# Kernel optimization log

Measured on AMD Instinct MI355X. Metric: run time of the kernel, lower is better.

Reference implementation:

```python
import jax, jax.numpy as jnp
import numpy as np

N, E, H, C = 100000, 800000, 128, 26


def setup_inputs() -> dict:
    key = jax.random.key(0)
    ks = jax.random.split(key, 12)
    s = 0.05
    return {
        "node_feat": jax.random.normal(ks[0], (N, H), jnp.float32),
        "descriptor": jax.random.normal(ks[1], (N, H), jnp.float32),
        "sub_idx": jax.random.randint(ks[2], (E,), 0, N, jnp.int32),
        "obj_idx": jax.random.randint(ks[3], (E,), 0, N, jnp.int32),
        "We": jax.random.normal(ks[4], (2 * H, H), jnp.float32) * s,
        "be": jnp.zeros((H,), jnp.float32),
        "Wq": jax.random.normal(ks[5], (2 * H, H), jnp.float32) * s,
        "bq": jnp.zeros((H,), jnp.float32),
        "Wk": jax.random.normal(ks[6], (2 * H, H), jnp.float32) * s,
        "bk": jnp.zeros((H,), jnp.float32),
        "Wv": jax.random.normal(ks[7], (2 * H, H), jnp.float32) * s,
        "bv": jnp.zeros((H,), jnp.float32),
        "Wc1": jax.random.normal(ks[8], (H, H // 2), jnp.float32) * s,
        "bc1": jnp.zeros((H // 2,), jnp.float32),
        "Wc2": jax.random.normal(ks[9], (H // 2, H // 4), jnp.float32) * s,
        "bc2": jnp.zeros((H // 4,), jnp.float32),
        "Wc3": jax.random.normal(ks[10], (H // 4, C), jnp.float32) * s,
        "bc3": jnp.zeros((C,), jnp.float32),
    }


def reference(node_feat, descriptor, sub_idx, obj_idx,
              We, be, Wq, bq, Wk, bk, Wv, bv,
              Wc1, bc1, Wc2, bc2, Wc3, bc3):
    # Gather edge endpoint features (irregular access), concat -> [E, 2H]
    geo = jnp.concatenate([node_feat[sub_idx], node_feat[obj_idx]], axis=1)
    non_geo = jnp.concatenate([descriptor[sub_idx], descriptor[obj_idx]], axis=1)

    origin = geo @ We + be          # edge_lin
    query = geo @ Wq + bq
    key = non_geo @ Wk + bk
    value = non_geo @ Wv + bv

    # elementwise q*k then softmax over feature dim (dim=1 in torch)
    alpha = jax.nn.softmax(query * key, axis=1)
    fused = value * alpha + origin  # [E, H]

    # classifier: Linear+ReLU, Linear (no ReLU), Linear(->classes)
    h = jax.nn.relu(fused @ Wc1 + bc1)
    h = h @ Wc2 + bc2
    out = h @ Wc3 + bc3             # [E, C]
    return out
```

## Files before the change

### kernel.cpp

```cpp
#include <hip/hip_runtime.h>
#include <hip/hip_bf16.h>

typedef short short8 __attribute__((ext_vector_type(8)));
typedef float f32x4 __attribute__((ext_vector_type(4)));
typedef unsigned int uint4v __attribute__((ext_vector_type(4)));

#define NEDGE 800000
#define NNODE 100000
#define HD    128
#define TM    64
#define LDA   264
#define LDF   136
#define LDH1  72
#define LDH2  40

#define WOFF_NFB   142336
#define WOFF_DESCB (142336 + 12800000)
#define WS_NEED    ((size_t)(142336 + 2 * 12800000) * 2)

__device__ __forceinline__ unsigned short f2bf(float f) {
    unsigned int u = __float_as_uint(f);
    unsigned int r = u + 0x7fffu + ((u >> 16) & 1u);
    return (unsigned short)(r >> 16);
}
__device__ __forceinline__ float bf2f(unsigned short u) {
    union { unsigned int i; float f; } v; v.i = ((unsigned int)u) << 16; return v.f;
}
__device__ __forceinline__ unsigned int pk_bf16(float a, float b) {
    __hip_bfloat162 h = __float22bfloat162_rn(make_float2(a, b));
    union { __hip_bfloat162 h2; unsigned int u; } c; c.h2 = h; return c.u;
}

__global__ void pack_convert(const float* __restrict__ We, const float* __restrict__ Wq,
                             const float* __restrict__ Wk, const float* __restrict__ Wv,
                             const float* __restrict__ Wc1, const float* __restrict__ Wc2,
                             const float* __restrict__ Wc3,
                             const float* __restrict__ nf, const float* __restrict__ desc,
                             unsigned short* __restrict__ ws) {
    int b = blockIdx.x;
    if (b >= 556) {
        int cb = b - 556;
        const float* src; unsigned short* dst;
        if (cb < 6250) { src = nf;   dst = ws + WOFF_NFB; }
        else           { src = desc; dst = ws + WOFF_DESCB; cb -= 6250; }
        long i = ((long)cb * 256 + threadIdx.x) * 8;
        f32x4 v0 = *(const f32x4*)(src + i);
        f32x4 v1 = *(const f32x4*)(src + i + 4);
        uint4v o;
        o.x = pk_bf16(v0[0], v0[1]);
        o.y = pk_bf16(v0[2], v0[3]);
        o.z = pk_bf16(v1[0], v1[1]);
        o.w = pk_bf16(v1[2], v1[3]);
        *(uint4v*)(dst + i) = o;
        return;
    }
    const float* src; unsigned short* dst; int KT, NT, ncols;
    if (b < 512) {
        int sel = b >> 7;
        src = sel == 0 ? We : sel == 1 ? Wq : sel == 2 ? Wk : Wv;
        dst = ws + sel * 32768;
        KT = 8; NT = 8; ncols = 128; b &= 127;
    } else if (b < 544) { src = Wc1; dst = ws + 131072; KT = 4; NT = 4; ncols = 64; b -= 512; }
    else if (b < 552)   { src = Wc2; dst = ws + 139264; KT = 2; NT = 2; ncols = 32; b -= 544; }
    else                { src = Wc3; dst = ws + 141312; KT = 1; NT = 2; ncols = 26; b -= 552; }
    int idx = b * 256 + threadIdx.x;
    int total = NT * KT * 64 * 8;
    if (idx >= total) return;
    int j = idx & 7;
    int l = (idx >> 3) & 63;
    int rem = idx >> 9;
    int s = rem % KT;
    int t = rem / KT;
    int k = s * 32 + ((l >> 4) << 3) + j;
    int n = t * 16 + (l & 15);
    dst[idx] = (n < ncols) ? f2bf(src[k * ncols + n]) : (unsigned short)0;
}

template<bool TAB>
__global__ __launch_bounds__(256, 4)
void fused_relcls(const float* __restrict__ nf,
                  const float* __restrict__ desc,
                  const int* __restrict__ sub, const int* __restrict__ obj,
                  const unsigned short* __restrict__ nfb, const unsigned short* __restrict__ descb,
                  const unsigned short* __restrict__ wef, const unsigned short* __restrict__ wqf,
                  const unsigned short* __restrict__ wkf, const unsigned short* __restrict__ wvf,
                  const unsigned short* __restrict__ wc1f, const unsigned short* __restrict__ wc2f,
                  const unsigned short* __restrict__ wc3f,
                  const float* __restrict__ be, const float* __restrict__ bq,
                  const float* __restrict__ bk, const float* __restrict__ bv,
                  const float* __restrict__ bc1, const float* __restrict__ bc2,
                  const float* __restrict__ bc3,
                  float* __restrict__ out)
{
    __shared__ __align__(16) unsigned short Abuf[TM * LDA];
    __shared__ float ssm[TM * 4];
    unsigned short* h1Buf = Abuf + 8704;
    unsigned short* h2Buf = Abuf + 13312;

    const int t  = threadIdx.x;
    const int w  = t >> 6;
    const int l  = t & 63;
    const int cl = l & 15;
    const int cq = l >> 4;
    const long e0 = (long)blockIdx.x * TM;
    const int wu = __builtin_amdgcn_readfirstlane(w);
    const int half = l >> 5;
    const int ci   = l & 31;

    if constexpr (TAB) {
        #pragma unroll
        for (int i = 0; i < 16; ++i) {
            int e = wu + 4 * i;
            int idx = half ? obj[e0 + e] : sub[e0 + e];
            uint2 g = *(const uint2*)(nfb + (long)idx * HD + ci * 4);
            *(uint2*)&Abuf[e * LDA + half * HD + ci * 4] = g;
        }
    } else {
        #pragma unroll
        for (int i = 0; i < 16; ++i) {
            int e = wu + 4 * i;
            int si = sub[e0 + e];
            int oi = obj[e0 + e];
            int idx = half ? oi : si;
            f32x4 v = *(const f32x4*)(nf + (long)idx * HD + ci * 4);
            uint2 o;
            o.x = pk_bf16(v[0], v[1]);
            o.y = pk_bf16(v[2], v[3]);
            *(uint2*)&Abuf[e * LDA + half * HD + ci * 4] = o;
        }
    }
    __syncthreads();

    f32x4 acc0[4][2], acc1[4][2];
    unsigned int opk[16];

    {
        float b0 = be[w * 32 + cl], b1 = be[w * 32 + 16 + cl];
        #pragma unroll
        for (int m = 0; m < 4; ++m) {
            acc0[m][0] = (f32x4){b0, b0, b0, b0};
            acc0[m][1] = (f32x4){b1, b1, b1, b1};
        }
        #pragma unroll
        for (int ks = 0; ks < 8; ++ks) {
            short8 a[4];
            #pragma unroll
            for (int m = 0; m < 4; ++m)
                a[m] = *(const short8*)&Abuf[(m * 16 + cl) * LDA + ks * 32 + cq * 8];
            short8 bw[2];
            #pragma unroll
            for (int tt = 0; tt < 2; ++tt)
                bw[tt] = *(const short8*)&wef[(((w * 2 + tt) * 8 + ks) * 64 + l) * 8];
            #pragma unroll
            for (int m = 0; m < 4; ++m)
                #pragma unroll
                for (int tt = 0; tt < 2; ++tt)
                    acc0[m][tt] = __builtin_amdgcn_mfma_f32_16x16x32_bf16(a[m], bw[tt], acc0[m][tt], 0, 0, 0);
        }
        #pragma unroll
        for (int m = 0; m < 4; ++m)
            #pragma unroll
            for (int tt = 0; tt < 2; ++tt) {
                opk[m * 4 + tt * 2 + 0] = pk_bf16(acc0[m][tt][0], acc0[m][tt][1]);
                opk[m * 4 + tt * 2 + 1] = pk_bf16(acc0[m][tt][2], acc0[m][tt][3]);
            }
    }

    {
        float b0 = bq[w * 32 + cl], b1 = bq[w * 32 + 16 + cl];
        #pragma unroll
        for (int m = 0; m < 4; ++m) {
            acc0[m][0] = (f32x4){b0, b0, b0, b0};
            acc0[m][1] = (f32x4){b1, b1, b1, b1};
        }
        #pragma unroll
        for (int ks = 0; ks < 8; ++ks) {
            short8 a[4];
            #pragma unroll
            for (int m = 0; m < 4; ++m)
                a[m] = *(const short8*)&Abuf[(m * 16 + cl) * LDA + ks * 32 + cq * 8];
            short8 bw[2];
            #pragma unroll
            for (int tt = 0; tt < 2; ++tt)
                bw[tt] = *(const short8*)&wqf[(((w * 2 + tt) * 8 + ks) * 64 + l) * 8];
            #pragma unroll
            for (int m = 0; m < 4; ++m)
                #pragma unroll
                for (int tt = 0; tt < 2; ++tt)
                    acc0[m][tt] = __builtin_amdgcn_mfma_f32_16x16x32_bf16(a[m], bw[tt], acc0[m][tt], 0, 0, 0);
        }
    }
    __syncthreads();

    if constexpr (TAB) {
        #pragma unroll
        for (int i = 0; i < 16; ++i) {
            int e = wu + 4 * i;
            int idx = half ? obj[e0 + e] : sub[e0 + e];
            uint2 g = *(const uint2*)(descb + (long)idx * HD + ci * 4);
            *(uint2*)&Abuf[e * LDA + half * HD + ci * 4] = g;
        }
    } else {
        #pragma unroll
        for (int i = 0; i < 16; ++i) {
            int e = wu + 4 * i;
            int si = sub[e0 + e];
            int oi = obj[e0 + e];
            int idx = half ? oi : si;
            f32x4 v = *(const f32x4*)(desc + (long)idx * HD + ci * 4);
            uint2 o;
            o.x = pk_bf16(v[0], v[1]);
            o.y = pk_bf16(v[2], v[3]);
            *(uint2*)&Abuf[e * LDA + half * HD + ci * 4] = o;
        }
    }
    __syncthreads();

    {
        float b0 = bk[w * 32 + cl], b1 = bk[w * 32 + 16 + cl];
        #pragma unroll
        for (int m = 0; m < 4; ++m) {
            acc1[m][0] = (f32x4){b0, b0, b0, b0};
            acc1[m][1] = (f32x4){b1, b1, b1, b1};
        }
        #pragma unroll
        for (int ks = 0; ks < 8; ++ks) {
            short8 a[4];
            #pragma unroll
            for (int m = 0; m < 4; ++m)
                a[m] = *(const short8*)&Abuf[(m * 16 + cl) * LDA + ks * 32 + cq * 8];
            short8 bw[2];
            #pragma unroll
            for (int tt = 0; tt < 2; ++tt)
                bw[tt] = *(const short8*)&wkf[(((w * 2 + tt) * 8 + ks) * 64 + l) * 8];
            #pragma unroll
            for (int m = 0; m < 4; ++m)
                #pragma unroll
                for (int tt = 0; tt < 2; ++tt)
                    acc1[m][tt] = __builtin_amdgcn_mfma_f32_16x16x32_bf16(a[m], bw[tt], acc1[m][tt], 0, 0, 0);
        }
        #pragma unroll
        for (int m = 0; m < 4; ++m)
            #pragma unroll
            for (int tt = 0; tt < 2; ++tt)
                acc0[m][tt] *= acc1[m][tt];
    }

    {
        #pragma unroll
        for (int m = 0; m < 4; ++m) {
            float es[4];
            #pragma unroll
            for (int r = 0; r < 4; ++r) {
                float ea = __expf(acc0[m][0][r]);
                float eb = __expf(acc0[m][1][r]);
                acc0[m][0][r] = ea;
                acc0[m][1][r] = eb;
                float s = ea + eb;
                s += __shfl_xor(s, 1);
                s += __shfl_xor(s, 2);
                s += __shfl_xor(s, 4);
                s += __shfl_xor(s, 8);
                es[r] = s;
            }
            if (cl == 0) {
                #pragma unroll
                for (int r = 0; r < 4; ++r)
                    ssm[(m * 16 + cq * 4 + r) * 4 + w] = es[r];
            }
        }
    }

    {
        float b0 = bv[w * 32 + cl], b1 = bv[w * 32 + 16 + cl];
        #pragma unroll
        for (int m = 0; m < 4; ++m) {
            acc1[m][0] = (f32x4){b0, b0, b0, b0};
            acc1[m][1] = (f32x4){b1, b1, b1, b1};
        }
        #pragma unroll
        for (int ks = 0; ks < 8; ++ks) {
            short8 a[4];
            #pragma unroll
            for (int m = 0; m < 4; ++m)
                a[m] = *(const short8*)&Abuf[(m * 16 + cl) * LDA + ks * 32 + cq * 8];
            short8 bw[2];
            #pragma unroll
            for (int tt = 0; tt < 2; ++tt)
                bw[tt] = *(const short8*)&wvf[(((w * 2 + tt) * 8 + ks) * 64 + l) * 8];
            #pragma unroll
            for (int m = 0; m < 4; ++m)
                #pragma unroll
                for (int tt = 0; tt < 2; ++tt)
                    acc1[m][tt] = __builtin_amdgcn_mfma_f32_16x16x32_bf16(a[m], bw[tt], acc1[m][tt], 0, 0, 0);
        }
    }
    __syncthreads();

    {
        unsigned short* fusedBuf = Abuf;
        #pragma unroll
        for (int m = 0; m < 4; ++m)
            #pragma unroll
            for (int r = 0; r < 4; ++r) {
                int row = m * 16 + cq * 4 + r;
                f32x4 b = *(const f32x4*)&ssm[row * 4];
                float inv = 1.0f / (b[0] + b[1] + b[2] + b[3]);
                #pragma unroll
                for (int tt = 0; tt < 2; ++tt) {
                    unsigned int word = opk[m * 4 + tt * 2 + (r >> 1)];
                    unsigned short us = (r & 1) ? (unsigned short)(word >> 16) : (unsigned short)(word & 0xffffu);
                    float Oval = bf2f(us);
                    float alpha = acc0[m][tt][r] * inv;
                    float f = acc1[m][tt][r] * alpha + Oval;
                    fusedBuf[row * LDF + w * 32 + tt * 16 + cl] = f2bf(f);
                }
            }
    }
    __syncthreads();

    {
        const unsigned short* fusedBuf = Abuf;
        float b1 = bc1[w * 16 + cl];
        f32x4 acc[4];
        #pragma unroll
        for (int m = 0; m < 4; ++m) acc[m] = (f32x4){b1, b1, b1, b1};
        #pragma unroll
        for (int ks = 0; ks < 4; ++ks) {
            short8 a[4];
            #pragma unroll
            for (int m = 0; m < 4; ++m)
                a[m] = *(const short8*)&fusedBuf[(m * 16 + cl) * LDF + ks * 32 + cq * 8];
            short8 bw = *(const short8*)&wc1f[((w * 4 + ks) * 64 + l) * 8];
            #pragma unroll
            for (int m = 0; m < 4; ++m)
                acc[m] = __builtin_amdgcn_mfma_f32_16x16x32_bf16(a[m], bw, acc[m], 0, 0, 0);
        }
        #pragma unroll
        for (int m = 0; m < 4; ++m)
            #pragma unroll
            for (int r = 0; r < 4; ++r)
                h1Buf[(m * 16 + cq * 4 + r) * LDH1 + w * 16 + cl] = f2bf(fmaxf(acc[m][r], 0.f));
    }
    __syncthreads();

    {
        int tn = w & 1, mh = w >> 1;
        float b2 = bc2[tn * 16 + cl];
        f32x4 acc[2];
        acc[0] = (f32x4){b2, b2, b2, b2};
        acc[1] = (f32x4){b2, b2, b2, b2};
        #pragma unroll
        for (int ks = 0; ks < 2; ++ks) {
            short8 a[2];
            #pragma unroll
            for (int mm = 0; mm < 2; ++mm)
                a[mm] = *(const short8*)&h1Buf[((mh * 2 + mm) * 16 + cl) * LDH1 + ks * 32 + cq * 8];
            short8 bw = *(const short8*)&wc2f[((tn * 2 + ks) * 64 + l) * 8];
            #pragma unroll
            for (int mm = 0; mm < 2; ++mm)
                acc[mm] = __builtin_amdgcn_mfma_f32_16x16x32_bf16(a[mm], bw, acc[mm], 0, 0, 0);
        }
        #pragma unroll
        for (int mm = 0; mm < 2; ++mm)
            #pragma unroll
            for (int r = 0; r < 4; ++r)
                h2Buf[((mh * 2 + mm) * 16 + cq * 4 + r) * LDH2 + tn * 16 + cl] = f2bf(acc[mm][r]);
    }
    __syncthreads();

    {
        f32x4 acc[2];
        #pragma unroll
        for (int tt = 0; tt < 2; ++tt) {
            int col = tt * 16 + cl;
            float b3 = (col < 26) ? bc3[col] : 0.f;
            acc[tt] = (f32x4){b3, b3, b3, b3};
        }
        short8 a = *(const short8*)&h2Buf[(w * 16 + cl) * LDH2 + cq * 8];
        #pragma unroll
        for (int tt = 0; tt < 2; ++tt)
            acc[tt] = __builtin_amdgcn_mfma_f32_16x16x32_bf16(a, *(const short8*)&wc3f[(tt * 64 + l) * 8], acc[tt], 0, 0, 0);
        float* ostg = (float*)Abuf;
        #pragma unroll
        for (int tt = 0; tt < 2; ++tt) {
            int col = tt * 16 + cl;
            if (col < 26) {
                #pragma unroll
                for (int r = 0; r < 4; ++r)
                    ostg[(w * 16 + cq * 4 + r) * 26 + col] = acc[tt][r];
            }
        }
    }
    __syncthreads();

    {
        const uint4v* src = (const uint4v*)Abuf;
        uint4v* dst = (uint4v*)(out + e0 * 26);
        #pragma unroll
        for (int k2 = 0; k2 < 2; ++k2) {
            int idx = t + k2 * 256;
            if (idx < 416)
                dst[idx] = src[idx];
        }
    }
}

extern "C" void kernel_launch(void* const* d_in, const int* in_sizes, int n_in,
                              void* d_out, int out_size, void* d_ws, size_t ws_size,
                              hipStream_t stream) {
    const float* nf   = (const float*)d_in[0];
    const float* desc = (const float*)d_in[1];
    const int* sub = (const int*)d_in[2];
    const int* obj = (const int*)d_in[3];
    const float* We  = (const float*)d_in[4];
    const float* be  = (const float*)d_in[5];
    const float* Wq  = (const float*)d_in[6];
    const float* bq  = (const float*)d_in[7];
    const float* Wk  = (const float*)d_in[8];
    const float* bk  = (const float*)d_in[9];
    const float* Wv  = (const float*)d_in[10];
    const float* bv  = (const float*)d_in[11];
    const float* Wc1 = (const float*)d_in[12];
    const float* bc1 = (const float*)d_in[13];
    const float* Wc2 = (const float*)d_in[14];
    const float* bc2 = (const float*)d_in[15];
    const float* Wc3 = (const float*)d_in[16];
    const float* bc3 = (const float*)d_in[17];

    unsigned short* ws = (unsigned short*)d_ws;
    unsigned short* wef  = ws;
    unsigned short* wqf  = ws + 32768;
    unsigned short* wkf  = ws + 65536;
    unsigned short* wvf  = ws + 98304;
    unsigned short* wc1f = ws + 131072;
    unsigned short* wc2f = ws + 139264;
    unsigned short* wc3f = ws + 141312;
    unsigned short* nfb   = ws + WOFF_NFB;
    unsigned short* descb = ws + WOFF_DESCB;

    const bool tab = (ws_size >= WS_NEED);
    const int prep_grid = tab ? 13056 : 556;

    pack_convert<<<prep_grid, 256, 0, stream>>>(We, Wq, Wk, Wv, Wc1, Wc2, Wc3, nf, desc, ws);

    if (tab) {
        fused_relcls<true><<<NEDGE / TM, 256, 0, stream>>>(
            nf, desc, sub, obj, nfb, descb,
            wef, wqf, wkf, wvf, wc1f, wc2f, wc3f,
            be, bq, bk, bv, bc1, bc2, bc3,
            (float*)d_out);
    } else {
        fused_relcls<false><<<NEDGE / TM, 256, 0, stream>>>(
            nf, desc, sub, obj, nfb, descb,
            wef, wqf, wkf, wvf, wc1f, wc2f, wc3f,
            be, bq, bk, bv, bc1, bc2, bc3,
            (float*)d_out);
    }
}
```

Before: 513.1 us.

## Persistent grid with register prefetch of next tile's gathers and paired MFMA passes

Turns the fused edge kernel into a persistent kernel with a fixed grid that loops over tiles. The next tile's bf16 node_feat and descriptor rows are prefetched into registers while the current tile computes, so gather latency overlaps with MFMA work. Both feature sets are staged in one wider LDS buffer, and the E/Q and K/V projections are computed in paired passes, which removes the mid-kernel reload and barriers. The cost is more registers (occupancy hint lowered from 4 to 2 blocks), more LDS, and a pack kernel that launches twice as many blocks with half the work each.

```diff
diff --git a/kernel.cpp b/kernel.cpp
--- a/kernel.cpp
+++ b/kernel.cpp
@@ -9,10 +9,9 @@
 #define NNODE 100000
 #define HD    128
 #define TM    64
-#define LDA   264
-#define LDF   136
-#define LDH1  72
-#define LDH2  40
+#define NTILES (NEDGE / TM)
+#define GRID_P 1024
+#define LDA2  528
 
 #define WOFF_NFB   142336
 #define WOFF_DESCB (142336 + 12800000)
@@ -41,17 +40,14 @@
     if (b >= 556) {
         int cb = b - 556;
         const float* src; unsigned short* dst;
-        if (cb < 6250) { src = nf;   dst = ws + WOFF_NFB; }
-        else           { src = desc; dst = ws + WOFF_DESCB; cb -= 6250; }
-        long i = ((long)cb * 256 + threadIdx.x) * 8;
-        f32x4 v0 = *(const f32x4*)(src + i);
-        f32x4 v1 = *(const f32x4*)(src + i + 4);
-        uint4v o;
-        o.x = pk_bf16(v0[0], v0[1]);
-        o.y = pk_bf16(v0[2], v0[3]);
-        o.z = pk_bf16(v1[0], v1[1]);
-        o.w = pk_bf16(v1[2], v1[3]);
-        *(uint4v*)(dst + i) = o;
+        if (cb < 12500) { src = nf;   dst = ws + WOFF_NFB; }
+        else            { src = desc; dst = ws + WOFF_DESCB; cb -= 12500; }
+        long i = ((long)cb * 256 + threadIdx.x) * 4;
+        f32x4 v = *(const f32x4*)(src + i);
+        uint2 o;
+        o.x = pk_bf16(v[0], v[1]);
+        o.y = pk_bf16(v[2], v[3]);
+        *(uint2*)(dst + i) = o;
         return;
     }
     const float* src; unsigned short* dst; int KT, NT, ncols;
@@ -77,7 +73,7 @@
 }
 
 template<bool TAB>
-__global__ __launch_bounds__(256, 4)
+__global__ __launch_bounds__(256, 2)
 void fused_relcls(const float* __restrict__ nf,
                   const float* __restrict__ desc,
                   const int* __restrict__ sub, const int* __restrict__ obj,
@@ -92,317 +88,279 @@
                   const float* __restrict__ bc3,
                   float* __restrict__ out)
 {
-    __shared__ __align__(16) unsigned short Abuf[TM * LDA];
+    __shared__ __align__(16) unsigned short Abuf[TM * LDA2];
+    __shared__ __align__(16) unsigned short h2s[TM * 40];
+    __shared__ __align__(16) float ostg[TM * 26];
     __shared__ float ssm[TM * 4];
-    unsigned short* h1Buf = Abuf + 8704;
-    unsigned short* h2Buf = Abuf + 13312;
 
     const int t  = threadIdx.x;
     const int w  = t >> 6;
     const int l  = t & 63;
     const int cl = l & 15;
     const int cq = l >> 4;
-    const long e0 = (long)blockIdx.x * TM;
     const int wu = __builtin_amdgcn_readfirstlane(w);
     const int half = l >> 5;
     const int ci   = l & 31;
 
+    const float bO0 = be[w * 32 + cl], bO1 = be[w * 32 + 16 + cl];
+    const float bQ0 = bq[w * 32 + cl], bQ1 = bq[w * 32 + 16 + cl];
+    const float bK0 = bk[w * 32 + cl], bK1 = bk[w * 32 + 16 + cl];
+    const float bV0 = bv[w * 32 + cl], bV1 = bv[w * 32 + 16 + cl];
+    const float bC1 = bc1[w * 16 + cl];
+    const int   tn = w & 1, mh = w >> 1;
+    const float bC2 = bc2[tn * 16 + cl];
+    const int   col0 = cl, col1 = 16 + cl;
+    const float bC3a = bc3[col0];
+    const float bC3b = (col1 < 26) ? bc3[col1] : 0.f;
+
+    uint2 pre[32];
+
     if constexpr (TAB) {
+        long pe0 = (long)blockIdx.x * TM;
         #pragma unroll
         for (int i = 0; i < 16; ++i) {
             int e = wu + 4 * i;
-            int idx = half ? obj[e0 + e] : sub[e0 + e];
-            uint2 g = *(const uint2*)(nfb + (long)idx * HD + ci * 4);
-            *(uint2*)&Abuf[e * LDA + half * HD + ci * 4] = g;
-        }
-    } else {
-        #pragma unroll
-        for (int i = 0; i < 16; ++i) {
-            int e = wu + 4 * i;
-            int si = sub[e0 + e];
-            int oi = obj[e0 + e];
-            int idx = half ? oi : si;
-            f32x4 v = *(const f32x4*)(nf + (long)idx * HD + ci * 4);
-            uint2 o;
-            o.x = pk_bf16(v[0], v[1]);
-            o.y = pk_bf16(v[2], v[3]);
-            *(uint2*)&Abuf[e * LDA + half * HD + ci * 4] = o;
+            int idx = half ? obj[pe0 + e] : sub[pe0 + e];
+            pre[i]      = *(const uint2*)(nfb   + (long)idx * HD + ci * 4);
+            pre[16 + i] = *(const uint2*)(descb + (long)idx * HD + ci * 4);
         }
     }
-    __syncthreads();
-
-    f32x4 acc0[4][2], acc1[4][2];
-    unsigned int opk[16];
-
-    {
-        float b0 = be[w * 32 + cl], b1 = be[w * 32 + 16 + cl];
-        #pragma unroll
-        for (int m = 0; m < 4; ++m) {
-            acc0[m][0] = (f32x4){b0, b0, b0, b0};
-            acc0[m][1] = (f32x4){b1, b1, b1, b1};
-        }
-        #pragma unroll
-        for (int ks = 0; ks < 8; ++ks) {
-            short8 a[4];
+
+    for (int tile = blockIdx.x; tile < NTILES; tile += GRID_P) {
+        const long e0 = (long)tile * TM;
+
+        if constexpr (TAB) {
+            #pragma unroll
+            for (int i = 0; i < 16; ++i) {
+                int e = wu + 4 * i;
+                *(uint2*)&Abuf[e * LDA2 + half * HD + ci * 4]       = pre[i];
+                *(uint2*)&Abuf[e * LDA2 + 256 + half * HD + ci * 4] = pre[16 + i];
+            }
+        } else {
+            #pragma unroll
+            for (int i = 0; i < 16; ++i) {
+                int e = wu + 4 * i;
+                int idx = half ? obj[e0 + e] : sub[e0 + e];
+                f32x4 v = *(const f32x4*)(nf + (long)idx * HD + ci * 4);
+                uint2 o; o.x = pk_bf16(v[0], v[1]); o.y = pk_bf16(v[2], v[3]);
+                *(uint2*)&Abuf[e * LDA2 + half * HD + ci * 4] = o;
+                f32x4 v2 = *(const f32x4*)(desc + (long)idx * HD + ci * 4);
+                uint2 o2; o2.x = pk_bf16(v2[0], v2[1]); o2.y = pk_bf16(v2[2], v2[3]);
+                *(uint2*)&Abuf[e * LDA2 + 256 + half * HD + ci * 4] = o2;
+            }
+        }
+        __syncthreads();
+
+        if constexpr (TAB) {
+            int ptile = (tile + GRID_P < NTILES) ? (tile + GRID_P) : tile;
+            long pe0 = (long)ptile * TM;
+            #pragma unroll
+            for (int i = 0; i < 16; ++i) {
+                int e = wu + 4 * i;
+                int idx = half ? obj[pe0 + e] : sub[pe0 + e];
+                pre[i]      = *(const uint2*)(nfb   + (long)idx * HD + ci * 4);
+                pre[16 + i] = *(const uint2*)(descb + (long)idx * HD + ci * 4);
+            }
+        }
+
+        f32x4 accO[4][2], accQ[4][2];
+        unsigned int opk[16];
+
+        {
+            #pragma unroll
+            for (int m = 0; m < 4; ++m) {
+                accO[m][0] = (f32x4){bO0, bO0, bO0, bO0};
+                accO[m][1] = (f32x4){bO1, bO1, bO1, bO1};
+                accQ[m][0] = (f32x4){bQ0, bQ0, bQ0, bQ0};
+                accQ[m][1] = (f32x4){bQ1, bQ1, bQ1, bQ1};
+            }
+            #pragma unroll
+            for (int ks = 0; ks < 8; ++ks) {
+                short8 a[4];
+                #pragma unroll
+                for (int m = 0; m < 4; ++m)
+                    a[m] = *(const short8*)&Abuf[(m * 16 + cl) * LDA2 + ks * 32 + cq * 8];
+                short8 bwe[2], bwq[2];
+                #pragma unroll
+                for (int tt = 0; tt < 2; ++tt) {
+                    bwe[tt] = *(const short8*)&wef[(((w * 2 + tt) * 8 + ks) * 64 + l) * 8];
+                    bwq[tt] = *(const short8*)&wqf[(((w * 2 + tt) * 8 + ks) * 64 + l) * 8];
+                }
+                #pragma unroll
+                for (int m = 0; m < 4; ++m)
+                    #pragma unroll
+                    for (int tt = 0; tt < 2; ++tt) {
+                        accO[m][tt] = __builtin_amdgcn_mfma_f32_16x16x32_bf16(a[m], bwe[tt], accO[m][tt], 0, 0, 0);
+                        accQ[m][tt] = __builtin_amdgcn_mfma_f32_16x16x32_bf16(a[m], bwq[tt], accQ[m][tt], 0, 0, 0);
+                    }
+            }
             #pragma unroll
             for (int m = 0; m < 4; ++m)
-                a[m] = *(const short8*)&Abuf[(m * 16 + cl) * LDA + ks * 32 + cq * 8];
-            short8 bw[2];
-            #pragma unroll
-            for (int tt = 0; tt < 2; ++tt)
-                bw[tt] = *(const short8*)&wef[(((w * 2 + tt) * 8 + ks) * 64 + l) * 8];
+                #pragma unroll
+                for (int tt = 0; tt < 2; ++tt) {
+                    opk[m * 4 + tt * 2 + 0] = pk_bf16(accO[m][tt][0], accO[m][tt][1]);
+                    opk[m * 4 + tt * 2 + 1] = pk_bf16(accO[m][tt][2], accO[m][tt][3]);
+                }
+        }
+
+        f32x4 accK[4][2], accV[4][2];
+        {
+            #pragma unroll
+            for (int m = 0; m < 4; ++m) {
+                accK[m][0] = (f32x4){bK0, bK0, bK0, bK0};
+                accK[m][1] = (f32x4){bK1, bK1, bK1, bK1};
+                accV[m][0] = (f32x4){bV0, bV0, bV0, bV0};
+                accV[m][1] = (f32x4){bV1, bV1, bV1, bV1};
+            }
+            #pragma unroll
+            for (int ks = 0; ks < 8; ++ks) {
+                short8 a[4];
+                #pragma unroll
+                for (int m = 0; m < 4; ++m)
+                    a[m] = *(const short8*)&Abuf[(m * 16 + cl) * LDA2 + 256 + ks * 32 + cq * 8];
+                short8 bwk[2], bwv[2];
+                #pragma unroll
+                for (int tt = 0; tt < 2; ++tt) {
+                    bwk[tt] = *(const short8*)&wkf[(((w * 2 + tt) * 8 + ks) * 64 + l) * 8];
+                    bwv[tt] = *(const short8*)&wvf[(((w * 2 + tt) * 8 + ks) * 64 + l) * 8];
+                }
+                #pragma unroll
+                for (int m = 0; m < 4; ++m)
+                    #pragma unroll
+                    for (int tt = 0; tt < 2; ++tt) {
+                        accK[m][tt] = __builtin_amdgcn_mfma_f32_16x16x32_bf16(a[m], bwk[tt], accK[m][tt], 0, 0, 0);
+                        accV[m][tt] = __builtin_amdgcn_mfma_f32_16x16x32_bf16(a[m], bwv[tt], accV[m][tt], 0, 0, 0);
+                    }
+            }
             #pragma unroll
             for (int m = 0; m < 4; ++m)
                 #pragma unroll
                 for (int tt = 0; tt < 2; ++tt)
-                    acc0[m][tt] = __builtin_amdgcn_mfma_f32_16x16x32_bf16(a[m], bw[tt], acc0[m][tt], 0, 0, 0);
-        }
-        #pragma unroll
-        for (int m = 0; m < 4; ++m)
-            #pragma unroll
-            for (int tt = 0; tt < 2; ++tt) {
-                opk[m * 4 + tt * 2 + 0] = pk_bf16(acc0[m][tt][0], acc0[m][tt][1]);
-                opk[m * 4 + tt * 2 + 1] = pk_bf16(acc0[m][tt][2], acc0[m][tt][3]);
-            }
-    }
-
-    {
-        float b0 = bq[w * 32 + cl], b1 = bq[w * 32 + 16 + cl];
-        #pragma unroll
-        for (int m = 0; m < 4; ++m) {
-            acc0[m][0] = (f32x4){b0, b0, b0, b0};
-            acc0[m][1] = (f32x4){b1, b1, b1, b1};
-        }
-        #pragma unroll
-        for (int ks = 0; ks < 8; ++ks) {
-            short8 a[4];
+                    accQ[m][tt] *= accK[m][tt];
+        }
+
+        {
+            #pragma unroll
+            for (int m = 0; m < 4; ++m) {
+                float es[4];
+                #pragma unroll
+                for (int r = 0; r < 4; ++r) {
+                    float ea = __expf(accQ[m][0][r]);
+                    float eb = __expf(accQ[m][1][r]);
+                    accQ[m][0][r] = ea;
+                    accQ[m][1][r] = eb;
+                    float s = ea + eb;
+                    s += __shfl_xor(s, 1);
+                    s += __shfl_xor(s, 2);
+                    s += __shfl_xor(s, 4);
+                    s += __shfl_xor(s, 8);
+                    es[r] = s;
+                }
+                if (cl == 0) {
+                    #pragma unroll
+                    for (int r = 0; r < 4; ++r)
+                        ssm[(m * 16 + cq * 4 + r) * 4 + w] = es[r];
+                }
+            }
+        }
+        __syncthreads();
+
+        {
             #pragma unroll
             for (int m = 0; m < 4; ++m)
-                a[m] = *(const short8*)&Abuf[(m * 16 + cl) * LDA + ks * 32 + cq * 8];
-            short8 bw[2];
-            #pragma unroll
-            for (int tt = 0; tt < 2; ++tt)
-                bw[tt] = *(const short8*)&wqf[(((w * 2 + tt) * 8 + ks) * 64 + l) * 8];
+                #pragma unroll
+                for (int r = 0; r < 4; ++r) {
+                    int row = m * 16 + cq * 4 + r;
+                    f32x4 b = *(const f32x4*)&ssm[row * 4];
+                    float inv = 1.0f / (b[0] + b[1] + b[2] + b[3]);
+                    #pragma unroll
+                    for (int tt = 0; tt < 2; ++tt) {
+                        unsigned int word = opk[m * 4 + tt * 2 + (r >> 1)];
+                        unsigned short us = (r & 1) ? (unsigned short)(word >> 16) : (unsigned short)(word & 0xffffu);
+                        float Oval = bf2f(us);
+                        float alpha = accQ[m][tt][r] * inv;
+                        float f = accV[m][tt][r] * alpha + Oval;
+                        Abuf[row * LDA2 + w * 32 + tt * 16 + cl] = f2bf(f);
+                    }
+                }
+        }
+        __syncthreads();
+
+        {
+            f32x4 acc[4];
+            #pragma unroll
+            for (int m = 0; m < 4; ++m) acc[m] = (f32x4){bC1, bC1, bC1, bC1};
+            #pragma unroll
+            for (int ks = 0; ks < 4; ++ks) {
+                short8 a[4];
+                #pragma unroll
+                for (int m = 0; m < 4; ++m)
+                    a[m] = *(const short8*)&Abuf[(m * 16 + cl) * LDA2 + ks * 32 + cq * 8];
+                short8 bw = *(const short8*)&wc1f[((w * 4 + ks) * 64 + l) * 8];
+                #pragma unroll
+                for (int m = 0; m < 4; ++m)
+                    acc[m] = __builtin_amdgcn_mfma_f32_16x16x32_bf16(a[m], bw, acc[m], 0, 0, 0);
+            }
             #pragma unroll
             for (int m = 0; m < 4; ++m)
                 #pragma unroll
-                for (int tt = 0; tt < 2; ++tt)
-                    acc0[m][tt] = __builtin_amdgcn_mfma_f32_16x16x32_bf16(a[m], bw[tt], acc0[m][tt], 0, 0, 0);
-        }
-    }
-    __syncthreads();
-
-    if constexpr (TAB) {
-        #pragma unroll
-        for (int i = 0; i < 16; ++i) {
-            int e = wu + 4 * i;
-            int idx = half ? obj[e0 + e] : sub[e0 + e];
-            uint2 g = *(const uint2*)(descb + (long)idx * HD + ci * 4);
-            *(uint2*)&Abuf[e * LDA + half * HD + ci * 4] = g;
-        }
-    } else {
-        #pragma unroll
-        for (int i = 0; i < 16; ++i) {
-            int e = wu + 4 * i;
-            int si = sub[e0 + e];
-            int oi = obj[e0 + e];
-            int idx = half ? oi : si;
-            f32x4 v = *(const f32x4*)(desc + (long)idx * HD + ci * 4);
-            uint2 o;
-            o.x = pk_bf16(v[0], v[1]);
-            o.y = pk_bf16(v[2], v[3]);
-            *(uint2*)&Abuf[e * LDA + half * HD + ci * 4] = o;
-        }
-    }
-    __syncthreads();
-
-    {
-        float b0 = bk[w * 32 + cl], b1 = bk[w * 32 + 16 + cl];
-        #pragma unroll
-        for (int m = 0; m < 4; ++m) {
-            acc1[m][0] = (f32x4){b0, b0, b0, b0};
-            acc1[m][1] = (f32x4){b1, b1, b1, b1};
-        }
-        #pragma unroll
-        for (int ks = 0; ks < 8; ++ks) {
-            short8 a[4];
-            #pragma unroll
-            for (int m = 0; m < 4; ++m)
-                a[m] = *(const short8*)&Abuf[(m * 16 + cl) * LDA + ks * 32 + cq * 8];
-            short8 bw[2];
-            #pragma unroll
-            for (int tt = 0; tt < 2; ++tt)
-                bw[tt] = *(const short8*)&wkf[(((w * 2 + tt) * 8 + ks) * 64 + l) * 8];
-            #pragma unroll
-            for (int m = 0; m < 4; ++m)
-                #pragma unroll
-                for (int tt = 0; tt < 2; ++tt)
-                    acc1[m][tt] = __builtin_amdgcn_mfma_f32_16x16x32_bf16(a[m], bw[tt], acc1[m][tt], 0, 0, 0);
-        }
-        #pragma unroll
-        for (int m = 0; m < 4; ++m)
-            #pragma unroll
-            for (int tt = 0; tt < 2; ++tt)
-                acc0[m][tt] *= acc1[m][tt];
-    }
-
-    {
-        #pragma unroll
-        for (int m = 0; m < 4; ++m) {
-            float es[4];
-            #pragma unroll
-            for (int r = 0; r < 4; ++r) {
-                float ea = __expf(acc0[m][0][r]);
-                float eb = __expf(acc0[m][1][r]);
-                acc0[m][0][r] = ea;
-                acc0[m][1][r] = eb;
-                float s = ea + eb;
-                s += __shfl_xor(s, 1);
-                s += __shfl_xor(s, 2);
-                s += __shfl_xor(s, 4);
-                s += __shfl_xor(s, 8);
-                es[r] = s;
-            }
-            if (cl == 0) {
-                #pragma unroll
                 for (int r = 0; r < 4; ++r)
-                    ssm[(m * 16 + cq * 4 + r) * 4 + w] = es[r];
-            }
-        }
-    }
-
-    {
-        float b0 = bv[w * 32 + cl], b1 = bv[w * 32 + 16 + cl];
-        #pragma unroll
-        for (int m = 0; m < 4; ++m) {
-            acc1[m][0] = (f32x4){b0, b0, b0, b0};
-            acc1[m][1] = (f32x4){b1, b1, b1, b1};
-        }
-        #pragma unroll
-        for (int ks = 0; ks < 8; ++ks) {
-            short8 a[4];
-            #pragma unroll
-            for (int m = 0; m < 4; ++m)
-                a[m] = *(const short8*)&Abuf[(m * 16 + cl) * LDA + ks * 32 + cq * 8];
-            short8 bw[2];
-            #pragma unroll
-            for (int tt = 0; tt < 2; ++tt)
-                bw[tt] = *(const short8*)&wvf[(((w * 2 + tt) * 8 + ks) * 64 + l) * 8];
-            #pragma unroll
-            for (int m = 0; m < 4; ++m)
-                #pragma unroll
-                for (int tt = 0; tt < 2; ++tt)
-                    acc1[m][tt] = __builtin_amdgcn_mfma_f32_16x16x32_bf16(a[m], bw[tt], acc1[m][tt], 0, 0, 0);
-        }
-    }
-    __syncthreads();
-
-    {
-        unsigned short* fusedBuf = Abuf;
-        #pragma unroll
-        for (int m = 0; m < 4; ++m)
-            #pragma unroll
-            for (int r = 0; r < 4; ++r) {
-                int row = m * 16 + cq * 4 + r;
-                f32x4 b = *(const f32x4*)&ssm[row * 4];
-                float inv = 1.0f / (b[0] + b[1] + b[2] + b[3]);
-                #pragma unroll
-                for (int tt = 0; tt < 2; ++tt) {
-                    unsigned int word = opk[m * 4 + tt * 2 + (r >> 1)];
-                    unsigned short us = (r & 1) ? (unsigned short)(word >> 16) : (unsigned short)(word & 0xffffu);
-                    float Oval = bf2f(us);
-                    float alpha = acc0[m][tt][r] * inv;
-                    float f = acc1[m][tt][r] * alpha + Oval;
-                    fusedBuf[row * LDF + w * 32 + tt * 16 + cl] = f2bf(f);
-                }
-            }
-    }
-    __syncthreads();
-
-    {
-        const unsigned short* fusedBuf = Abuf;
-        float b1 = bc1[w * 16 + cl];
-        f32x4 acc[4];
-        #pragma unroll
-        for (int m = 0; m < 4; ++m) acc[m] = (f32x4){b1, b1, b1, b1};
-        #pragma unroll
-        for (int ks = 0; ks < 4; ++ks) {
-            short8 a[4];
-            #pragma unroll
-            for (int m = 0; m < 4; ++m)
-                a[m] = *(const short8*)&fusedBuf[(m * 16 + cl) * LDF + ks * 32 + cq * 8];
-            short8 bw = *(const short8*)&wc1f[((w * 4 + ks) * 64 + l) * 8];
-            #pragma unroll
-            for (int m = 0; m < 4; ++m)
-                acc[m] = __builtin_amdgcn_mfma_f32_16x16x32_bf16(a[m], bw, acc[m], 0, 0, 0);
-        }
-        #pragma unroll
-        for (int m = 0; m < 4; ++m)
+                    Abuf[(m * 16 + cq * 4 + r) * LDA2 + 256 + w * 16 + cl] = f2bf(fmaxf(acc[m][r], 0.f));
+        }
+        __syncthreads();
+
+        {
+            f32x4 acc[2];
+            acc[0] = (f32x4){bC2, bC2, bC2, bC2};
+            acc[1] = (f32x4){bC2, bC2, bC2, bC2};
+            #pragma unroll
+            for (int ks = 0; ks < 2; ++ks) {
+                short8 a[2];
+                #pragma unroll
+                for (int mm = 0; mm < 2; ++mm)
+                    a[mm] = *(const short8*)&Abuf[((mh * 2 + mm) * 16 + cl) * LDA2 + 256 + ks * 32 + cq * 8];
+                short8 bw = *(const short8*)&wc2f[((tn * 2 + ks) * 64 + l) * 8];
+                #pragma unroll
+                for (int mm = 0; mm < 2; ++mm)
+                    acc[mm] = __builtin_amdgcn_mfma_f32_16x16x32_bf16(a[mm], bw, acc[mm], 0, 0, 0);
+            }
+            #pragma unroll
+            for (int mm = 0; mm < 2; ++mm)
+                #pragma unroll
+                for (int r = 0; r < 4; ++r)
+                    h2s[((mh * 2 + mm) * 16 + cq * 4 + r) * 40 + tn * 16 + cl] = f2bf(acc[mm][r]);
+        }
+        __syncthreads();
+
+        {
+            f32x4 acc[2];
+            acc[0] = (f32x4){bC3a, bC3a, bC3a, bC3a};
+            acc[1] = (f32x4){bC3b, bC3b, bC3b, bC3b};
+            short8 a = *(const short8*)&h2s[(w * 16 + cl) * 40 + cq * 8];
+            acc[0] = __builtin_amdgcn_mfma_f32_16x16x32_bf16(a, *(const short8*)&wc3f[(0 * 64 + l) * 8], acc[0], 0, 0, 0);
+            acc[1] = __builtin_amdgcn_mfma_f32_16x16x32_bf16(a, *(const short8*)&wc3f[(1 * 64 + l) * 8], acc[1], 0, 0, 0);
             #pragma unroll
             for (int r = 0; r < 4; ++r)
-                h1Buf[(m * 16 + cq * 4 + r) * LDH1 + w * 16 + cl] = f2bf(fmaxf(acc[m][r], 0.f));
-    }
-    __syncthreads();
-
-    {
-        int tn = w & 1, mh = w >> 1;
-        float b2 = bc2[tn * 16 + cl];
-        f32x4 acc[2];
-        acc[0] = (f32x4){b2, b2, b2, b2};
-        acc[1] = (f32x4){b2, b2, b2, b2};
-        #pragma unroll
-        for (int ks = 0; ks < 2; ++ks) {
-            short8 a[2];
-            #pragma unroll
-            for (int mm = 0; mm < 2; ++mm)
-                a[mm] = *(const short8*)&h1Buf[((mh * 2 + mm) * 16 + cl) * LDH1 + ks * 32 + cq * 8];
-            short8 bw = *(const short8*)&wc2f[((tn * 2 + ks) * 64 + l) * 8];
-            #pragma unroll
-            for (int mm = 0; mm < 2; ++mm)
-                acc[mm] = __builtin_amdgcn_mfma_f32_16x16x32_bf16(a[mm], bw, acc[mm], 0, 0, 0);
-        }
-        #pragma unroll
-        for (int mm = 0; mm < 2; ++mm)
-            #pragma unroll
-            for (int r = 0; r < 4; ++r)
-                h2Buf[((mh * 2 + mm) * 16 + cq * 4 + r) * LDH2 + tn * 16 + cl] = f2bf(acc[mm][r]);
-    }
-    __syncthreads();
-
-    {
-        f32x4 acc[2];
-        #pragma unroll
-        for (int tt = 0; tt < 2; ++tt) {
-            int col = tt * 16 + cl;
-            float b3 = (col < 26) ? bc3[col] : 0.f;
-            acc[tt] = (f32x4){b3, b3, b3, b3};
-        }
-        short8 a = *(const short8*)&h2Buf[(w * 16 + cl) * LDH2 + cq * 8];
-        #pragma unroll
-        for (int tt = 0; tt < 2; ++tt)
-            acc[tt] = __builtin_amdgcn_mfma_f32_16x16x32_bf16(a, *(const short8*)&wc3f[(tt * 64 + l) * 8], acc[tt], 0, 0, 0);
-        float* ostg = (float*)Abuf;
-        #pragma unroll
-        for (int tt = 0; tt < 2; ++tt) {
-            int col = tt * 16 + cl;
-            if (col < 26) {
+                ostg[(w * 16 + cq * 4 + r) * 26 + col0] = acc[0][r];
+            if (col1 < 26) {
                 #pragma unroll
                 for (int r = 0; r < 4; ++r)
-                    ostg[(w * 16 + cq * 4 + r) * 26 + col] = acc[tt][r];
-            }
-        }
-    }
-    __syncthreads();
-
-    {
-        const uint4v* src = (const uint4v*)Abuf;
-        uint4v* dst = (uint4v*)(out + e0 * 26);
-        #pragma unroll
-        for (int k2 = 0; k2 < 2; ++k2) {
-            int idx = t + k2 * 256;
-            if (idx < 416)
-                dst[idx] = src[idx];
-        }
+                    ostg[(w * 16 + cq * 4 + r) * 26 + col1] = acc[1][r];
+            }
+        }
+        __syncthreads();
+
+        {
+            const uint4v* src = (const uint4v*)ostg;
+            uint4v* dst = (uint4v*)(out + e0 * 26);
+            #pragma unroll
+            for (int k2 = 0; k2 < 2; ++k2) {
+                int idx = t + k2 * 256;
+                if (idx < 416)
+                    dst[idx] = src[idx];
+            }
+        }
+        __syncthreads();
     }
 }
 
@@ -440,18 +398,18 @@
     unsigned short* descb = ws + WOFF_DESCB;
 
     const bool tab = (ws_size >= WS_NEED);
-    const int prep_grid = tab ? 13056 : 556;
+    const int prep_grid = tab ? (556 + 25000) : 556;
 
     pack_convert<<<prep_grid, 256, 0, stream>>>(We, Wq, Wk, Wv, Wc1, Wc2, Wc3, nf, desc, ws);
 
     if (tab) {
-        fused_relcls<true><<<NEDGE / TM, 256, 0, stream>>>(
+        fused_relcls<true><<<GRID_P, 256, 0, stream>>>(
             nf, desc, sub, obj, nfb, descb,
             wef, wqf, wkf, wvf, wc1f, wc2f, wc3f,
             be, bq, bk, bv, bc1, bc2, bc3,
             (float*)d_out);
     } else {
-        fused_relcls<false><<<NEDGE / TM, 256, 0, stream>>>(
+        fused_relcls<false><<<GRID_P, 256, 0, stream>>>(
             nf, desc, sub, obj, nfb, descb,
             wef, wqf, wkf, wvf, wc1f, wc2f, wc3f,
             be, bq, bk, bv, bc1, bc2, bc3,
```

After: 1.245 ms. +142.7%, slower.

## Gather edge features directly into swizzled LDS via global_load_lds

Applied to the files above, without the earlier changes.

Replaces the register-staged gather of bf16 node/descriptor rows with direct global-to-LDS 16-byte loads, and switches the A tile from a padded row layout to two unpadded 64x128 halves with an XOR swizzle that keeps MFMA operand reads free of bank conflicts. All A-fragment reads are rewritten to use the swizzled addressing. The prep conversion kernel is also changed to launch twice as many blocks, each converting 4 floats per thread. This aims to cut VGPR use and gather latency, at the cost of more complex indexing and reliance on the LDS-direct load builtin.

```diff
diff --git a/kernel.cpp b/kernel.cpp
--- a/kernel.cpp
+++ b/kernel.cpp
@@ -9,7 +9,6 @@
 #define NNODE 100000
 #define HD    128
 #define TM    64
-#define LDA   264
 #define LDF   136
 #define LDH1  72
 #define LDH2  40
@@ -29,6 +28,11 @@
 __device__ __forceinline__ unsigned int pk_bf16(float a, float b) {
     __hip_bfloat162 h = __float22bfloat162_rn(make_float2(a, b));
     union { __hip_bfloat162 h2; unsigned int u; } c; c.h2 = h; return c.u;
+}
+__device__ __forceinline__ void gload_lds16(const unsigned short* g, unsigned short* lds) {
+    __builtin_amdgcn_global_load_lds(
+        (const __attribute__((address_space(1))) unsigned int*)g,
+        (__attribute__((address_space(3))) unsigned int*)lds, 16, 0, 0);
 }
 
 __global__ void pack_convert(const float* __restrict__ We, const float* __restrict__ Wq,
@@ -41,17 +45,14 @@
     if (b >= 556) {
         int cb = b - 556;
         const float* src; unsigned short* dst;
-        if (cb < 6250) { src = nf;   dst = ws + WOFF_NFB; }
-        else           { src = desc; dst = ws + WOFF_DESCB; cb -= 6250; }
-        long i = ((long)cb * 256 + threadIdx.x) * 8;
-        f32x4 v0 = *(const f32x4*)(src + i);
-        f32x4 v1 = *(const f32x4*)(src + i + 4);
-        uint4v o;
-        o.x = pk_bf16(v0[0], v0[1]);
-        o.y = pk_bf16(v0[2], v0[3]);
-        o.z = pk_bf16(v1[0], v1[1]);
-        o.w = pk_bf16(v1[2], v1[3]);
-        *(uint4v*)(dst + i) = o;
+        if (cb < 12500) { src = nf;   dst = ws + WOFF_NFB; }
+        else            { src = desc; dst = ws + WOFF_DESCB; cb -= 12500; }
+        long i = ((long)cb * 256 + threadIdx.x) * 4;
+        f32x4 v = *(const f32x4*)(src + i);
+        uint2 o;
+        o.x = pk_bf16(v[0], v[1]);
+        o.y = pk_bf16(v[2], v[3]);
+        *(uint2*)(dst + i) = o;
         return;
     }
     const float* src; unsigned short* dst; int KT, NT, ncols;
@@ -92,7 +93,7 @@
                   const float* __restrict__ bc3,
                   float* __restrict__ out)
 {
-    __shared__ __align__(16) unsigned short Abuf[TM * LDA];
+    __shared__ __align__(16) unsigned short Abuf[16384];
     __shared__ float ssm[TM * 4];
     unsigned short* h1Buf = Abuf + 8704;
     unsigned short* h2Buf = Abuf + 13312;
@@ -104,29 +105,40 @@
     const int cq = l >> 4;
     const long e0 = (long)blockIdx.x * TM;
     const int wu = __builtin_amdgcn_readfirstlane(w);
-    const int half = l >> 5;
-    const int ci   = l & 31;
+    const int rbase = wu * 16;
 
     if constexpr (TAB) {
-        #pragma unroll
-        for (int i = 0; i < 16; ++i) {
-            int e = wu + 4 * i;
-            int idx = half ? obj[e0 + e] : sub[e0 + e];
-            uint2 g = *(const uint2*)(nfb + (long)idx * HD + ci * 4);
-            *(uint2*)&Abuf[e * LDA + half * HD + ci * 4] = g;
+        int si4[4], oi4[4], cg4[4];
+        #pragma unroll
+        for (int g = 0; g < 4; ++g) {
+            int r = rbase + g * 4 + cq;
+            si4[g] = sub[e0 + r];
+            oi4[g] = obj[e0 + r];
+            cg4[g] = (cl ^ (r & 15)) << 3;
+        }
+        #pragma unroll
+        for (int g = 0; g < 4; ++g) {
+            gload_lds16(nfb + (long)si4[g] * HD + cg4[g], &Abuf[(rbase + g * 4) * 128]);
+            gload_lds16(nfb + (long)oi4[g] * HD + cg4[g], &Abuf[8192 + (rbase + g * 4) * 128]);
         }
     } else {
         #pragma unroll
-        for (int i = 0; i < 16; ++i) {
-            int e = wu + 4 * i;
-            int si = sub[e0 + e];
-            int oi = obj[e0 + e];
-            int idx = half ? oi : si;
-            f32x4 v = *(const f32x4*)(nf + (long)idx * HD + ci * 4);
-            uint2 o;
-            o.x = pk_bf16(v[0], v[1]);
-            o.y = pk_bf16(v[2], v[3]);
-            *(uint2*)&Abuf[e * LDA + half * HD + ci * 4] = o;
+        for (int g = 0; g < 4; ++g) {
+            int r = rbase + g * 4 + cq;
+            int si = sub[e0 + r], oi = obj[e0 + r];
+            int cgf = (cl ^ (r & 15)) << 3;
+            f32x4 v0 = *(const f32x4*)(nf + (long)si * HD + cgf);
+            f32x4 v1 = *(const f32x4*)(nf + (long)si * HD + cgf + 4);
+            uint4v o;
+            o.x = pk_bf16(v0[0], v0[1]); o.y = pk_bf16(v0[2], v0[3]);
+            o.z = pk_bf16(v1[0], v1[1]); o.w = pk_bf16(v1[2], v1[3]);
+            *(uint4v*)&Abuf[r * 128 + cl * 8] = o;
+            f32x4 u0 = *(const f32x4*)(nf + (long)oi * HD + cgf);
+            f32x4 u1 = *(const f32x4*)(nf + (long)oi * HD + cgf + 4);
+            uint4v o2;
+            o2.x = pk_bf16(u0[0], u0[1]); o2.y = pk_bf16(u0[2], u0[3]);
+            o2.z = pk_bf16(u1[0], u1[1]); o2.w = pk_bf16(u1[2], u1[3]);
+            *(uint4v*)&Abuf[8192 + r * 128 + cl * 8] = o2;
         }
     }
     __syncthreads();
@@ -143,10 +155,12 @@
         }
         #pragma unroll
         for (int ks = 0; ks < 8; ++ks) {
+            const unsigned short* pl = Abuf + ((ks < 4) ? 0 : 8192);
+            const int ch = ((((ks & 3) << 2) | cq) ^ cl) << 3;
             short8 a[4];
             #pragma unroll
             for (int m = 0; m < 4; ++m)
-                a[m] = *(const short8*)&Abuf[(m * 16 + cl) * LDA + ks * 32 + cq * 8];
+                a[m] = *(const short8*)&pl[(m * 16 + cl) * 128 + ch];
             short8 bw[2];
             #pragma unroll
             for (int tt = 0; tt < 2; ++tt)
@@ -175,10 +189,12 @@
         }
         #pragma unroll
         for (int ks = 0; ks < 8; ++ks) {
+            const unsigned short* pl = Abuf + ((ks < 4) ? 0 : 8192);
+            const int ch = ((((ks & 3) << 2) | cq) ^ cl) << 3;
             short8 a[4];
             #pragma unroll
             for (int m = 0; m < 4; ++m)
-                a[m] = *(const short8*)&Abuf[(m * 16 + cl) * LDA + ks * 32 + cq * 8];
+                a[m] = *(const short8*)&pl[(m * 16 + cl) * 128 + ch];
             short8 bw[2];
             #pragma unroll
             for (int tt = 0; tt < 2; ++tt)
@@ -193,25 +209,37 @@
     __syncthreads();
 
     if constexpr (TAB) {
-        #pragma unroll
-        for (int i = 0; i < 16; ++i) {
-            int e = wu + 4 * i;
-            int idx = half ? obj[e0 + e] : sub[e0 + e];
-            uint2 g = *(const uint2*)(descb + (long)idx * HD + ci * 4);
-            *(uint2*)&Abuf[e * LDA + half * HD + ci * 4] = g;
+        int si4[4], oi4[4], cg4[4];
+        #pragma unroll
+        for (int g = 0; g < 4; ++g) {
+            int r = rbase + g * 4 + cq;
+            si4[g] = sub[e0 + r];
+            oi4[g] = obj[e0 + r];
+            cg4[g] = (cl ^ (r & 15)) << 3;
+        }
+        #pragma unroll
+        for (int g = 0; g < 4; ++g) {
+            gload_lds16(descb + (long)si4[g] * HD + cg4[g], &Abuf[(rbase + g * 4) * 128]);
+            gload_lds16(descb + (long)oi4[g] * HD + cg4[g], &Abuf[8192 + (rbase + g * 4) * 128]);
         }
     } else {
         #pragma unroll
-        for (int i = 0; i < 16; ++i) {
-            int e = wu + 4 * i;
-            int si = sub[e0 + e];
-            int oi = obj[e0 + e];
-            int idx = half ? oi : si;
-            f32x4 v = *(const f32x4*)(desc + (long)idx * HD + ci * 4);
-            uint2 o;
-            o.x = pk_bf16(v[0], v[1]);
-            o.y = pk_bf16(v[2], v[3]);
-            *(uint2*)&Abuf[e * LDA + half * HD + ci * 4] = o;
+        for (int g = 0; g < 4; ++g) {
+            int r = rbase + g * 4 + cq;
+            int si = sub[e0 + r], oi = obj[e0 + r];
+            int cgf = (cl ^ (r & 15)) << 3;
+            f32x4 v0 = *(const f32x4*)(desc + (long)si * HD + cgf);
+            f32x4 v1 = *(const f32x4*)(desc + (long)si * HD + cgf + 4);
+            uint4v o;
+            o.x = pk_bf16(v0[0], v0[1]); o.y = pk_bf16(v0[2], v0[3]);
+            o.z = pk_bf16(v1[0], v1[1]); o.w = pk_bf16(v1[2], v1[3]);
+            *(uint4v*)&Abuf[r * 128 + cl * 8] = o;
+            f32x4 u0 = *(const f32x4*)(desc + (long)oi * HD + cgf);
+            f32x4 u1 = *(const f32x4*)(desc + (long)oi * HD + cgf + 4);
+            uint4v o2;
+            o2.x = pk_bf16(u0[0], u0[1]); o2.y = pk_bf16(u0[2], u0[3]);
+            o2.z = pk_bf16(u1[0], u1[1]); o2.w = pk_bf16(u1[2], u1[3]);
+            *(uint4v*)&Abuf[8192 + r * 128 + cl * 8] = o2;
         }
     }
     __syncthreads();
@@ -225,10 +253,12 @@
         }
         #pragma unroll
         for (int ks = 0; ks < 8; ++ks) {
+            const unsigned short* pl = Abuf + ((ks < 4) ? 0 : 8192);
+            const int ch = ((((ks & 3) << 2) | cq) ^ cl) << 3;
             short8 a[4];
             #pragma unroll
             for (int m = 0; m < 4; ++m)
-                a[m] = *(const short8*)&Abuf[(m * 16 + cl) * LDA + ks * 32 + cq * 8];
+                a[m] = *(const short8*)&pl[(m * 16 + cl) * 128 + ch];
             short8 bw[2];
             #pragma unroll
             for (int tt = 0; tt < 2; ++tt)
@@ -280,10 +310,12 @@
         }
         #pragma unroll
         for (int ks = 0; ks < 8; ++ks) {
+            const unsigned short* pl = Abuf + ((ks < 4) ? 0 : 8192);
+            const int ch = ((((ks & 3) << 2) | cq) ^ cl) << 3;
             short8 a[4];
             #pragma unroll
             for (int m = 0; m < 4; ++m)
-                a[m] = *(const short8*)&Abuf[(m * 16 + cl) * LDA + ks * 32 + cq * 8];
+                a[m] = *(const short8*)&pl[(m * 16 + cl) * 128 + ch];
             short8 bw[2];
             #pragma unroll
             for (int tt = 0; tt < 2; ++tt)
@@ -440,7 +472,7 @@
     unsigned short* descb = ws + WOFF_DESCB;
 
     const bool tab = (ws_size >= WS_NEED);
-    const int prep_grid = tab ? 13056 : 556;
+    const int prep_grid = tab ? (556 + 25000) : 556;
 
     pack_convert<<<prep_grid, 256, 0, stream>>>(We, Wq, Wk, Wv, Wc1, Wc2, Wc3, nf, desc, ws);
 
```

Measured after the change: 552.2 us. 1.08x slower.
